# Kernel tuning notes

Hardware: AMD Instinct MI355X
Metric: run time of the kernel (lower is better)

## Reference

```python
import jax, jax.numpy as jnp
import numpy as np
import math

N_EMBD = 1024
N_HEAD = 16
BLOCK_SIZE = 1024
B, T = 4, 1024


def setup_inputs() -> dict:
    key = jax.random.key(0)
    ks = jax.random.split(key, 7)
    C = N_EMBD
    # torch Linear weights stored here as [in, out] so y = x @ W + b
    return {
        "x": jax.random.normal(ks[0], (B, T, C), dtype=jnp.float32),
        "Wqk": jax.random.normal(ks[1], (C, 2 * C), dtype=jnp.float32) * 0.02,
        "bqk": jnp.zeros((2 * C,), dtype=jnp.float32),
        "Wgate": jax.random.normal(ks[2], (C, N_HEAD), dtype=jnp.float32) * 0.02,
        "bgate": jnp.zeros((N_HEAD,), dtype=jnp.float32),
        "Wproj": jax.random.normal(ks[3], (C, C), dtype=jnp.float32) * 0.02,
        "bproj": jnp.zeros((C,), dtype=jnp.float32),
    }


def reference(x, Wqk, bqk, Wgate, bgate, Wproj, bproj):
    Bx, Tx, C = x.shape
    H = N_HEAD
    D = C // H
    # per-head geometrically shrinking causal windows (static, from init args)
    windows = jnp.array([max(4, BLOCK_SIZE // (2 ** h)) for h in range(H)], dtype=jnp.int32)

    qk = x @ Wqk + bqk                      # [B,T,2C]
    q, k = jnp.split(qk, 2, axis=-1)
    v = k                                   # module sets v = k chunk

    # [B,H,T,D]
    q = q.reshape(Bx, Tx, H, D).transpose(0, 2, 1, 3)
    k = k.reshape(Bx, Tx, H, D).transpose(0, 2, 1, 3)
    v = v.reshape(Bx, Tx, H, D).transpose(0, 2, 1, 3)

    i = jnp.arange(Tx)[:, None]
    j = jnp.arange(Tx)[None, :]
    # mask[h,i,j] = causal AND within window: j in [i-window+1, i]
    mask = (j <= i)[None] & (j > i - windows[:, None, None])   # [H,T,T]

    att = jnp.einsum("bhtd,bhsd->bhts", q, k) * (1.0 / math.sqrt(D))
    att = jnp.where(mask[None], att, -jnp.inf)
    att = jax.nn.softmax(att, axis=-1)      # diagonal always unmasked -> safe

    out = jnp.einsum("bhts,bhsd->bhtd", att, v)   # [B,H,T,D]
    combined = out.transpose(0, 2, 1, 3)          # [B,T,H,D]

    gates = jax.nn.softmax(x @ Wgate + bgate, axis=-1)    # [B,T,H]
    gated = (combined * gates[..., None]).reshape(Bx, Tx, C)
    return gated @ Wproj + bproj
```

## Files before the change

kernel.cpp:

```cpp
#include <hip/hip_runtime.h>

typedef __attribute__((ext_vector_type(8))) short bf16x8;
typedef __attribute__((ext_vector_type(4))) float f32x4;

#define T_SEQ 1024
#define NH 16
#define CEMB 1024

__device__ __forceinline__ float asf(unsigned int u){ union{unsigned int i;float f;}x; x.i=u; return x.f; }
__device__ __forceinline__ float bf2f(unsigned short u){ return asf(((unsigned int)u)<<16); }
__device__ __forceinline__ unsigned short f2bf(float f){
  union{float f;unsigned int i;}x; x.f=f;
  unsigned int r = x.i + 0x7FFFu + ((x.i>>16)&1u);
  return (unsigned short)(r>>16);
}
__device__ __forceinline__ f32x4 MFMA16(bf16x8 a, bf16x8 b, f32x4 c){
  return __builtin_amdgcn_mfma_f32_16x16x32_bf16(a, b, c, 0,0,0);
}

__global__ void cvt_bf16_kernel(const float* __restrict__ in, unsigned short* __restrict__ out, int n){
  int i = (blockIdx.x*blockDim.x + threadIdx.x)*4;
  if (i >= n) return;
  float4 v = *reinterpret_cast<const float4*>(in + i);
  ushort4 o; o.x=f2bf(v.x); o.y=f2bf(v.y); o.z=f2bf(v.z); o.w=f2bf(v.w);
  *reinterpret_cast<ushort4*>(out + i) = o;
}

__global__ void gates_kernel(const float* __restrict__ x, const float* __restrict__ Wg,
                             const float* __restrict__ bg, float* __restrict__ gates){
  const int lane = threadIdx.x & 63;
  const int row  = blockIdx.x*4 + (threadIdx.x>>6);
  const float* xr = x + (size_t)row*CEMB;
  float acc[NH];
  #pragma unroll
  for (int h=0;h<NH;h++) acc[h]=0.f;
  for (int i=0;i<CEMB/64;i++){
    float xv = xr[i*64 + lane];
    const float4* wg = reinterpret_cast<const float4*>(Wg + (size_t)(i*64+lane)*NH);
    float4 a=wg[0], b=wg[1], c=wg[2], d=wg[3];
    acc[0]+=xv*a.x; acc[1]+=xv*a.y; acc[2]+=xv*a.z; acc[3]+=xv*a.w;
    acc[4]+=xv*b.x; acc[5]+=xv*b.y; acc[6]+=xv*b.z; acc[7]+=xv*b.w;
    acc[8]+=xv*c.x; acc[9]+=xv*c.y; acc[10]+=xv*c.z; acc[11]+=xv*c.w;
    acc[12]+=xv*d.x; acc[13]+=xv*d.y; acc[14]+=xv*d.z; acc[15]+=xv*d.w;
  }
  #pragma unroll
  for (int h=0;h<NH;h++){
    #pragma unroll
    for (int m=32;m;m>>=1) acc[h] += __shfl_xor(acc[h], m, 64);
  }
  float mx = -1e30f;
  #pragma unroll
  for (int h=0;h<NH;h++){ acc[h] += bg[h]; mx = fmaxf(mx, acc[h]); }
  float s = 0.f;
  #pragma unroll
  for (int h=0;h<NH;h++){ acc[h] = __expf(acc[h]-mx); s += acc[h]; }
  float g = 0.f;
  #pragma unroll
  for (int h=0;h<NH;h++) g = (lane==h) ? acc[h]/s : g;
  if (lane < NH) gates[(size_t)row*NH + lane] = g;
}

__global__ void wtrans_kernel(const float* __restrict__ Wqk, unsigned short* __restrict__ WqkT,
                              const float* __restrict__ Wproj, unsigned short* __restrict__ WprojT){
  __shared__ float tile[32][33];
  int blk = blockIdx.x;
  const float* W; unsigned short* Wt; int R, C, bx, by;
  if (blk < 2048){ W = Wqk;   Wt = WqkT;   R = 1024; C = 2048; bx = blk & 63; by = blk >> 6; }
  else { blk -= 2048; W = Wproj; Wt = WprojT; R = 1024; C = 1024; bx = blk & 31; by = blk >> 5; }
  const int c0 = bx*32, r0 = by*32;
  const int tx = threadIdx.x, ty = threadIdx.y;
  #pragma unroll
  for (int i=0;i<32;i+=8) tile[ty+i][tx] = W[(size_t)(r0+ty+i)*C + c0 + tx];
  __syncthreads();
  #pragma unroll
  for (int i=0;i<32;i+=8) Wt[(size_t)(c0+ty+i)*R + r0 + tx] = f2bf(tile[tx][ty+i]);
}

template<bool OUT_BF16, int BM>
__global__ __launch_bounds__(256)
void gemm_bt_kernel(const unsigned short* __restrict__ A, const unsigned short* __restrict__ Bt,
                    const float* __restrict__ bias, void* __restrict__ Cptr,
                    int M, int N, int K){
  constexpr int WCN   = (BM==128) ? 2 : 4;
  constexpr int MFRAG = (BM==128) ? 4 : 4;
  constexpr int NFRAG = 4/(WCN/2);
  constexpr int WCW   = 128/WCN;
  constexpr int AISS  = BM/32;
  __shared__ unsigned short lA0[BM*64], lA1[BM*64];
  __shared__ unsigned short lB0[128*64], lB1[128*64];
  const int tid = threadIdx.x;
  const int wid = tid>>6, lane = tid&63;
  const int nbm = M/BM;
  const int bid = blockIdx.x;
  const int bm = bid % nbm, bn = bid / nbm;
  const int wr = (BM==128) ? (wid>>1) : 0;
  const int wc = (BM==128) ? (wid&1) : wid;
  f32x4 acc[MFRAG][NFRAG] = {};

  const unsigned short* gA = A + (size_t)bm*BM*K;
  const unsigned short* gB = Bt + (size_t)bn*128*K;
  const int srow = lane>>3;
  const int schunk = lane&7;

#define GSTAGE(LA, LB, KK) do { \
  _Pragma("unroll") \
  for (int i_=0;i_<AISS;i_++){ \
    int rowi_ = (wid*AISS+i_)*8 + srow; \
    int cc_ = schunk ^ (rowi_ & 7); \
    __builtin_amdgcn_global_load_lds((const __attribute__((address_space(1))) void*)(gA + (size_t)rowi_*K + (KK) + cc_*8), \
        (__attribute__((address_space(3))) void*)&LA[(wid*AISS+i_)*512], 16, 0, 0); \
  } \
  _Pragma("unroll") \
  for (int i_=0;i_<4;i_++){ \
    int rowi_ = (wid*4+i_)*8 + srow; \
    int cc_ = schunk ^ (rowi_ & 7); \
    __builtin_amdgcn_global_load_lds((const __attribute__((address_space(1))) void*)(gB + (size_t)rowi_*K + (KK) + cc_*8), \
        (__attribute__((address_space(3))) void*)&LB[(wid*4+i_)*512], 16, 0, 0); \
  } \
} while(0)

#define GCOMPUTE(LA, LB) do { \
  _Pragma("unroll") \
  for (int ks_=0; ks_<2; ks_++){ \
    bf16x8 af_[MFRAG], bf_[NFRAG]; \
    _Pragma("unroll") \
    for (int m_=0;m_<MFRAG;m_++){ \
      int r_ = wr*64 + m_*16 + (lane&15); \
      int p_ = (ks_*4 + (lane>>4)) ^ (r_&7); \
      af_[m_] = *reinterpret_cast<const bf16x8*>(&LA[r_*64 + p_*8]); \
    } \
    _Pragma("unroll") \
    for (int n_=0;n_<NFRAG;n_++){ \
      int r_ = wc*WCW + n_*16 + (lane&15); \
      int p_ = (ks_*4 + (lane>>4)) ^ (r_&7); \
      bf_[n_] = *reinterpret_cast<const bf16x8*>(&LB[r_*64 + p_*8]); \
    } \
    _Pragma("unroll") \
    for (int m_=0;m_<MFRAG;m_++) \
      _Pragma("unroll") \
      for (int n_=0;n_<NFRAG;n_++) \
        acc[m_][n_] = __builtin_amdgcn_mfma_f32_16x16x32_bf16(af_[m_], bf_[n_], acc[m_][n_], 0,0,0); \
  } \
} while(0)

  GSTAGE(lA0, lB0, 0);
  __syncthreads();
  for (int k0=0; k0<K; k0+=128){
    GSTAGE(lA1, lB1, k0+64);
    GCOMPUTE(lA0, lB0);
    __syncthreads();
    if (k0+128 < K) GSTAGE(lA0, lB0, k0+128);
    GCOMPUTE(lA1, lB1);
    __syncthreads();
  }
#undef GSTAGE
#undef GCOMPUTE

  const int rq = lane>>4;
  const int cl = lane&15;
  #pragma unroll
  for (int n=0;n<NFRAG;n++){
    int col = bn*128 + wc*WCW + n*16 + cl;
    float bv = bias[col];
    #pragma unroll
    for (int m=0;m<MFRAG;m++){
      int row = bm*BM + wr*64 + m*16 + rq*4;
      #pragma unroll
      for (int r=0;r<4;r++){
        float v = acc[m][n][r] + bv;
        if (OUT_BF16) ((unsigned short*)Cptr)[(size_t)(row+r)*N + col] = f2bf(v);
        else          ((float*)Cptr)[(size_t)(row+r)*N + col] = v;
      }
    }
  }
}

__global__ __launch_bounds__(256)
void kpack_kernel(const unsigned short* __restrict__ qk,
                  unsigned short* __restrict__ Kpack, unsigned short* __restrict__ Vpack){
  __shared__ unsigned short lT[64][68];
  const int blk = blockIdx.x;
  const int t0 = (blk & 15) * 64;
  const int bh = blk >> 4;
  const int b = bh >> 4, h = bh & 15;
  const int tid = threadIdx.x;
  #pragma unroll
  for (int it=0; it<2; it++){
    int idx = tid + it*256;
    int row = idx >> 3, c = idx & 7;
    uint4 v = *reinterpret_cast<const uint4*>(qk + ((size_t)(b*T_SEQ + t0 + row)*2048 + 1024 + h*64 + c*8));
    *reinterpret_cast<uint4*>(&lT[row][c*8]) = v;
  }
  __syncthreads();
  const int wid = tid>>6, lane = tid&63;
  const int g = lane>>4, li = lane&15;
  const int tile = wid>>1;
  const int kt = (t0>>5) + tile;
  #pragma unroll
  for (int ff=0; ff<2; ff++){
    const int f = (wid&1)*2 + ff;
    const int row = tile*32 + ((f>>1)<<4) + li;
    const int col = (f&1)*32 + g*8;
    uint4 v = *reinterpret_cast<const uint4*>(&lT[row][col]);
    *reinterpret_cast<uint4*>(Kpack + ((((size_t)bh*32 + kt)*4 + f)*64 + lane)*8) = v;
  }
  #pragma unroll
  for (int ff=0; ff<2; ff++){
    const int d4 = (wid&1)*2 + ff;
    unsigned short vv[8];
    #pragma unroll
    for (int j=0;j<8;j++) vv[j] = lT[tile*32 + g*8 + j][d4*16 + li];
    *reinterpret_cast<uint4*>(Vpack + ((((size_t)bh*32 + kt)*4 + d4)*64 + lane)*8) = *reinterpret_cast<const uint4*>(vv);
  }
}

__global__ __launch_bounds__(256)
void attn_mfma_kernel(const unsigned short* __restrict__ qk,
                      const unsigned short* __restrict__ Kpack,
                      const unsigned short* __restrict__ Vpack,
                      const float* __restrict__ gates, unsigned short* __restrict__ gated,
                      unsigned short* __restrict__ pO, float* __restrict__ pL){
  __shared__ unsigned short lP[4][16*40];
  const int tid = threadIdx.x;
  const int wid = tid>>6, lane = tid&63;
  const int g = lane>>4, li = lane&15;

  const int W = blockIdx.x*4 + wid;
  int h, c, b, qw16; bool partial;
  if (W < 1024){ h = 0; c = W>>8; int r = W&255; b = r>>6; qw16 = r&63; partial = true; }
  else if (W < 1536){ h = 1; int Wp = W-1024; c = Wp>>8; int r = Wp&255; b = r>>6; qw16 = r&63; partial = true; }
  else { int Wp = W-1536; h = 2 + (Wp>>8); int r = Wp&255; b = r>>6; qw16 = r&63; c = 0; partial = false; }

  int w = 1024 >> h; if (w < 4) w = 4;
  const int qw0 = qw16*16;
  const int bh = b*NH + h;

  int mylo = qw0 - w + 1; if (mylo < 0) mylo = 0;
  const int kt_lo_full = mylo >> 5;
  const int kt_hi_full = (qw0 + 15) >> 5;
  const int slot = (b*64 + qw16)*6 + ((h==0) ? c : 4 + c);

  int kt_start, kt_end;
  if (partial){
    const int CH = (h==0) ? 8 : 9;
    kt_end = kt_hi_full - c*CH;
    kt_start = kt_end - (CH-1); if (kt_start < kt_lo_full) kt_start = kt_lo_full;
    if (kt_end < kt_lo_full){
      unsigned short* po = pO + (size_t)slot*16*64;
      #pragma unroll
      for (int r2=0;r2<4;r2++){
        const int row = g*4 + r2;
        #pragma unroll
        for (int d4=0; d4<4; d4++) po[row*64 + d4*16 + li] = 0;
      }
      if (li == 0){
        #pragma unroll
        for (int r2=0;r2<4;r2++) pL[(size_t)slot*16 + g*4 + r2] = 0.f;
      }
      return;
    }
  } else {
    kt_start = kt_lo_full; kt_end = kt_hi_full;
  }

  const unsigned short* qbase = qk + ((size_t)(b*T_SEQ + qw0 + li)*2048 + h*64 + g*8);
  const bf16x8 aq0 = *reinterpret_cast<const bf16x8*>(qbase);
  const bf16x8 aq1 = *reinterpret_cast<const bf16x8*>(qbase + 32);

  f32x4 oacc[4] = {};
  float lsum[4] = {0.f,0.f,0.f,0.f};

  const unsigned short* kp = Kpack + (size_t)bh*32*4*512;
  const unsigned short* vp = Vpack + (size_t)bh*32*4*512;
  const int loff = lane*8;

  bf16x8 kf[4], kn[4], bv[4];
  #pragma unroll
  for (int f=0; f<4; f++)
    kf[f] = *reinterpret_cast<const bf16x8*>(kp + (kt_start*4 + f)*512 + loff);

  for (int kt = kt_start; kt <= kt_end; ++kt){
    #pragma unroll
    for (int d4=0; d4<4; d4++)
      bv[d4] = *reinterpret_cast<const bf16x8*>(vp + (kt*4 + d4)*512 + loff);
    {
      const int ktn = (kt < kt_end) ? kt+1 : kt_end;
      #pragma unroll
      for (int f=0; f<4; f++)
        kn[f] = *reinterpret_cast<const bf16x8*>(kp + (ktn*4 + f)*512 + loff);
    }

    f32x4 s0 = {}, s1 = {};
    s0 = MFMA16(aq0, kf[0], s0);
    s0 = MFMA16(aq1, kf[1], s0);
    s1 = MFMA16(aq0, kf[2], s1);
    s1 = MFMA16(aq1, kf[3], s1);

    const int k0 = kt*32;
    #pragma unroll
    for (int r=0;r<4;r++){
      const int t = qw0 + g*4 + r;
      const int ka = k0 + li;
      const int kb2 = ka + 16;
      const bool v0 = (ka <= t) && (ka > t - w);
      const bool v1 = (kb2 <= t) && (kb2 > t - w);
      const float p0 = v0 ? __expf(s0[r]*0.125f) : 0.f;
      const float p1 = v1 ? __expf(s1[r]*0.125f) : 0.f;
      lsum[r] += p0 + p1;
      const int q = g*4 + r;
      lP[wid][q*40 + li]      = f2bf(p0);
      lP[wid][q*40 + 16 + li] = f2bf(p1);
    }
    const bf16x8 pa = *reinterpret_cast<const bf16x8*>(&lP[wid][li*40 + g*8]);
    #pragma unroll
    for (int d4=0; d4<4; d4++)
      oacc[d4] = MFMA16(pa, bv[d4], oacc[d4]);
    #pragma unroll
    for (int i=0;i<4;i++) kf[i] = kn[i];
  }

  #pragma unroll
  for (int msk=1; msk<16; msk<<=1){
    #pragma unroll
    for (int r=0;r<4;r++) lsum[r] += __shfl_xor(lsum[r], msk, 64);
  }

  if (partial){
    unsigned short* po = pO + (size_t)slot*16*64;
    #pragma unroll
    for (int r2=0;r2<4;r2++){
      const int row = g*4 + r2;
      #pragma unroll
      for (int d4=0; d4<4; d4++) po[row*64 + d4*16 + li] = f2bf(oacc[d4][r2]);
    }
    if (li == 0){
      #pragma unroll
      for (int r2=0;r2<4;r2++) pL[(size_t)slot*16 + g*4 + r2] = lsum[r2];
    }
  } else {
    #pragma unroll
    for (int r=0;r<4;r++){
      const int t = qw0 + g*4 + r;
      const float gv = gates[(size_t)(b*T_SEQ + t)*NH + h];
      const float inv = gv / lsum[r];
      unsigned short* orow = gated + (size_t)(b*T_SEQ + t)*CEMB + h*64 + li;
      orow[0]  = f2bf(oacc[0][r]*inv);
      orow[16] = f2bf(oacc[1][r]*inv);
      orow[32] = f2bf(oacc[2][r]*inv);
      orow[48] = f2bf(oacc[3][r]*inv);
    }
  }
}

__global__ __launch_bounds__(256)
void attn_merge_kernel(const unsigned short* __restrict__ pO, const float* __restrict__ pL,
                       const float* __restrict__ gates, unsigned short* __restrict__ gated){
  const int wid = threadIdx.x>>6, lane = threadIdx.x&63;
  const int W = blockIdx.x*4 + wid;
  const int h = W>>8;
  const int r = W&255;
  const int b = r>>6, qw16 = r&63;
  const int nch = (h==0) ? 4 : 2;
  const int sb  = (h==0) ? 0 : 4;
  const int slot0 = (b*64 + qw16)*6 + sb;
  for (int row=0; row<16; ++row){
    const int t = qw16*16 + row;
    float L = 0.f, acc = 0.f;
    #pragma unroll
    for (int c2=0;c2<4;c2++){
      if (c2 < nch){
        L   += pL[(size_t)(slot0+c2)*16 + row];
        acc += bf2f(pO[((size_t)(slot0+c2)*16 + row)*64 + lane]);
      }
    }
    const float gv = gates[(size_t)(b*T_SEQ + t)*NH + h];
    gated[(size_t)(b*T_SEQ + t)*CEMB + h*64 + lane] = f2bf(acc * gv / L);
  }
}

extern "C" void kernel_launch(void* const* d_in, const int* in_sizes, int n_in,
                              void* d_out, int out_size, void* d_ws, size_t ws_size,
                              hipStream_t stream){
  const float* x     = (const float*)d_in[0];
  const float* Wqk   = (const float*)d_in[1];
  const float* bqk   = (const float*)d_in[2];
  const float* Wgate = (const float*)d_in[3];
  const float* bgate = (const float*)d_in[4];
  const float* Wproj = (const float*)d_in[5];
  const float* bproj = (const float*)d_in[6];
  float* out = (float*)d_out;

  unsigned short* x_bf   = (unsigned short*)d_ws;
  unsigned short* WqkT   = x_bf   + (size_t)4096*1024;
  unsigned short* WprojT = WqkT   + (size_t)2048*1024;
  unsigned short* qkb    = WprojT + (size_t)1024*1024;
  unsigned short* gated  = qkb    + (size_t)4096*2048;
  float*          gates  = (float*)(gated + (size_t)4096*1024);
  unsigned short* pO     = WqkT;
  float*          pL     = (float*)(WqkT + (size_t)4*64*6*16*64);
  unsigned short* Kpack  = (unsigned short*)((char*)d_ws + (size_t)40*1024*1024);
  unsigned short* Vpack  = Kpack + (size_t)64*32*4*512;

  cvt_bf16_kernel<<<4096, 256, 0, stream>>>(x, x_bf, 4096*1024);
  wtrans_kernel<<<3072, dim3(32,8), 0, stream>>>(Wqk, WqkT, Wproj, WprojT);
  gates_kernel<<<1024, 256, 0, stream>>>(x, Wgate, bgate, gates);

  gemm_bt_kernel<true, 128><<<512, 256, 0, stream>>>(x_bf,  WqkT,   bqk,   qkb, 4096, 2048, 1024);
  kpack_kernel<<<1024, 256, 0, stream>>>(qkb, Kpack, Vpack);
  attn_mfma_kernel<<<1280, 256, 0, stream>>>(qkb, Kpack, Vpack, gates, gated, pO, pL);
  attn_merge_kernel<<<128, 256, 0, stream>>>(pO, pL, gates, gated);
  gemm_bt_kernel<false, 64><<<512, 256, 0, stream>>>(gated, WprojT, bproj, out, 4096, 1024, 1024);
}
```

Baseline: 110.9 us.

## Remove split-K partial chunks and merge kernel from windowed attention

```diff
diff --git a/kernel.cpp b/kernel.cpp
--- a/kernel.cpp
+++ b/kernel.cpp
@@ -82,7 +82,7 @@
                     const float* __restrict__ bias, void* __restrict__ Cptr,
                     int M, int N, int K){
   constexpr int WCN   = (BM==128) ? 2 : 4;
-  constexpr int MFRAG = (BM==128) ? 4 : 4;
+  constexpr int MFRAG = 4;
   constexpr int NFRAG = 4/(WCN/2);
   constexpr int WCW   = 128/WCN;
   constexpr int AISS  = BM/32;
@@ -218,50 +218,24 @@
 void attn_mfma_kernel(const unsigned short* __restrict__ qk,
                       const unsigned short* __restrict__ Kpack,
                       const unsigned short* __restrict__ Vpack,
-                      const float* __restrict__ gates, unsigned short* __restrict__ gated,
-                      unsigned short* __restrict__ pO, float* __restrict__ pL){
+                      const float* __restrict__ gates, unsigned short* __restrict__ gated){
   __shared__ unsigned short lP[4][16*40];
   const int tid = threadIdx.x;
   const int wid = tid>>6, lane = tid&63;
   const int g = lane>>4, li = lane&15;
 
-  const int W = blockIdx.x*4 + wid;
-  int h, c, b, qw16; bool partial;
-  if (W < 1024){ h = 0; c = W>>8; int r = W&255; b = r>>6; qw16 = r&63; partial = true; }
-  else if (W < 1536){ h = 1; int Wp = W-1024; c = Wp>>8; int r = Wp&255; b = r>>6; qw16 = r&63; partial = true; }
-  else { int Wp = W-1536; h = 2 + (Wp>>8); int r = Wp&255; b = r>>6; qw16 = r&63; c = 0; partial = false; }
+  const int V = wid*1024 + blockIdx.x;
+  const int h = V>>8;
+  const int rr = V&255;
+  const int b = rr>>6, qw16 = rr&63;
 
   int w = 1024 >> h; if (w < 4) w = 4;
   const int qw0 = qw16*16;
   const int bh = b*NH + h;
 
   int mylo = qw0 - w + 1; if (mylo < 0) mylo = 0;
-  const int kt_lo_full = mylo >> 5;
-  const int kt_hi_full = (qw0 + 15) >> 5;
-  const int slot = (b*64 + qw16)*6 + ((h==0) ? c : 4 + c);
-
-  int kt_start, kt_end;
-  if (partial){
-    const int CH = (h==0) ? 8 : 9;
-    kt_end = kt_hi_full - c*CH;
-    kt_start = kt_end - (CH-1); if (kt_start < kt_lo_full) kt_start = kt_lo_full;
-    if (kt_end < kt_lo_full){
-      unsigned short* po = pO + (size_t)slot*16*64;
-      #pragma unroll
-      for (int r2=0;r2<4;r2++){
-        const int row = g*4 + r2;
-        #pragma unroll
-        for (int d4=0; d4<4; d4++) po[row*64 + d4*16 + li] = 0;
-      }
-      if (li == 0){
-        #pragma unroll
-        for (int r2=0;r2<4;r2++) pL[(size_t)slot*16 + g*4 + r2] = 0.f;
-      }
-      return;
-    }
-  } else {
-    kt_start = kt_lo_full; kt_end = kt_hi_full;
-  }
+  const int kt_start = mylo >> 5;
+  const int kt_end = (qw0 + 15) >> 5;
 
   const unsigned short* qbase = qk + ((size_t)(b*T_SEQ + qw0 + li)*2048 + h*64 + g*8);
   const bf16x8 aq0 = *reinterpret_cast<const bf16x8*>(qbase);
@@ -325,56 +299,16 @@
     for (int r=0;r<4;r++) lsum[r] += __shfl_xor(lsum[r], msk, 64);
   }
 
-  if (partial){
-    unsigned short* po = pO + (size_t)slot*16*64;
-    #pragma unroll
-    for (int r2=0;r2<4;r2++){
-      const int row = g*4 + r2;
-      #pragma unroll
-      for (int d4=0; d4<4; d4++) po[row*64 + d4*16 + li] = f2bf(oacc[d4][r2]);
-    }
-    if (li == 0){
-      #pragma unroll
-      for (int r2=0;r2<4;r2++) pL[(size_t)slot*16 + g*4 + r2] = lsum[r2];
-    }
-  } else {
-    #pragma unroll
-    for (int r=0;r<4;r++){
-      const int t = qw0 + g*4 + r;
-      const float gv = gates[(size_t)(b*T_SEQ + t)*NH + h];
-      const float inv = gv / lsum[r];
-      unsigned short* orow = gated + (size_t)(b*T_SEQ + t)*CEMB + h*64 + li;
-      orow[0]  = f2bf(oacc[0][r]*inv);
-      orow[16] = f2bf(oacc[1][r]*inv);
-      orow[32] = f2bf(oacc[2][r]*inv);
-      orow[48] = f2bf(oacc[3][r]*inv);
-    }
-  }
-}
-
-__global__ __launch_bounds__(256)
-void attn_merge_kernel(const unsigned short* __restrict__ pO, const float* __restrict__ pL,
-                       const float* __restrict__ gates, unsigned short* __restrict__ gated){
-  const int wid = threadIdx.x>>6, lane = threadIdx.x&63;
-  const int W = blockIdx.x*4 + wid;
-  const int h = W>>8;
-  const int r = W&255;
-  const int b = r>>6, qw16 = r&63;
-  const int nch = (h==0) ? 4 : 2;
-  const int sb  = (h==0) ? 0 : 4;
-  const int slot0 = (b*64 + qw16)*6 + sb;
-  for (int row=0; row<16; ++row){
-    const int t = qw16*16 + row;
-    float L = 0.f, acc = 0.f;
-    #pragma unroll
-    for (int c2=0;c2<4;c2++){
-      if (c2 < nch){
-        L   += pL[(size_t)(slot0+c2)*16 + row];
-        acc += bf2f(pO[((size_t)(slot0+c2)*16 + row)*64 + lane]);
-      }
-    }
+  #pragma unroll
+  for (int r=0;r<4;r++){
+    const int t = qw0 + g*4 + r;
     const float gv = gates[(size_t)(b*T_SEQ + t)*NH + h];
-    gated[(size_t)(b*T_SEQ + t)*CEMB + h*64 + lane] = f2bf(acc * gv / L);
+    const float inv = gv / lsum[r];
+    unsigned short* orow = gated + (size_t)(b*T_SEQ + t)*CEMB + h*64 + li;
+    orow[0]  = f2bf(oacc[0][r]*inv);
+    orow[16] = f2bf(oacc[1][r]*inv);
+    orow[32] = f2bf(oacc[2][r]*inv);
+    orow[48] = f2bf(oacc[3][r]*inv);
   }
 }
 
@@ -396,8 +330,6 @@
   unsigned short* qkb    = WprojT + (size_t)1024*1024;
   unsigned short* gated  = qkb    + (size_t)4096*2048;
   float*          gates  = (float*)(gated + (size_t)4096*1024);
-  unsigned short* pO     = WqkT;
-  float*          pL     = (float*)(WqkT + (size_t)4*64*6*16*64);
   unsigned short* Kpack  = (unsigned short*)((char*)d_ws + (size_t)40*1024*1024);
   unsigned short* Vpack  = Kpack + (size_t)64*32*4*512;
 
@@ -407,7 +339,6 @@
 
   gemm_bt_kernel<true, 128><<<512, 256, 0, stream>>>(x_bf,  WqkT,   bqk,   qkb, 4096, 2048, 1024);
   kpack_kernel<<<1024, 256, 0, stream>>>(qkb, Kpack, Vpack);
-  attn_mfma_kernel<<<1280, 256, 0, stream>>>(qkb, Kpack, Vpack, gates, gated, pO, pL);
-  attn_merge_kernel<<<128, 256, 0, stream>>>(pO, pL, gates, gated);
+  attn_mfma_kernel<<<1024, 256, 0, stream>>>(qkb, Kpack, Vpack, gates, gated);
   gemm_bt_kernel<false, 64><<<512, 256, 0, stream>>>(gated, WprojT, bproj, out, 4096, 1024, 1024);
 }
```

New measurement: 103.5 us. 6.7% less time.
